# Kernel tuning notes

Hardware: AMD Instinct MI355X
Metric: run time of the kernel (lower is better)

Reference implementation:

```python
import jax, jax.numpy as jnp
import numpy as np

B, T, I, H, L = 32, 512, 512, 512, 2


def _gru_layer(x, w_ih, w_hh, b_ih, b_hh, reverse):
    # x: [B, T, in] ; w_ih: [3H, in] ; w_hh: [3H, H] ; gate order (r, z, n) as in PyTorch
    Bh = x.shape[0]
    Hh = w_hh.shape[1]
    pre = jnp.einsum('bti,gi->btg', x, w_ih) + b_ih  # [B, T, 3H] input projections, done once
    if reverse:
        pre = pre[:, ::-1]
    pre_t = jnp.swapaxes(pre, 0, 1)  # [T, B, 3H]
    h0 = jnp.zeros((Bh, Hh), x.dtype)

    def step(h, gx):
        gh = h @ w_hh.T + b_hh  # [B, 3H]
        r = jax.nn.sigmoid(gx[:, :Hh] + gh[:, :Hh])
        z = jax.nn.sigmoid(gx[:, Hh:2 * Hh] + gh[:, Hh:2 * Hh])
        n = jnp.tanh(gx[:, 2 * Hh:] + r * gh[:, 2 * Hh:])
        h_new = (1.0 - z) * n + z * h
        return h_new, h_new

    h_last, ys = jax.lax.scan(step, h0, pre_t)
    ys = jnp.swapaxes(ys, 0, 1)  # [B, T, H]
    if reverse:
        ys = ys[:, ::-1]
    return ys, h_last


def _encoder(context, params):
    # params: list of (w_ih, w_hh, b_ih, b_hh, w_ih_r, w_hh_r, b_ih_r, b_hh_r) per layer
    x = context
    finals = []  # interleaved fwd, bwd per layer, like torch GRU's `final`
    for (w_ih, w_hh, b_ih, b_hh, w_ih_r, w_hh_r, b_ih_r, b_hh_r) in params:
        y_f, h_f = _gru_layer(x, w_ih, w_hh, b_ih, b_hh, reverse=False)
        y_b, h_b = _gru_layer(x, w_ih_r, w_hh_r, b_ih_r, b_hh_r, reverse=True)
        x = jnp.concatenate([y_f, y_b], axis=-1)  # [B, T, 2H]
        finals.append(h_f)
        finals.append(h_b)
    final = jnp.stack(finals, axis=0)  # [2L, B, H]
    fwd_final = final[0::2]  # [L, B, H]
    bwd_final = final[1::2]
    final = jnp.concatenate([fwd_final, bwd_final], axis=2)  # [L, B, 2H]
    return x, final


def setup_inputs() -> dict:
    key = jax.random.key(0)
    ks = jax.random.split(key, 20)
    s = 1.0 / np.sqrt(H)  # PyTorch-style uniform-ish scale
    d = {'context': jax.random.normal(ks[0], (B, T, I), jnp.float32)}
    shapes = {
        'w_ih_l0': (3 * H, I), 'w_hh_l0': (3 * H, H), 'b_ih_l0': (3 * H,), 'b_hh_l0': (3 * H,),
        'w_ih_l0r': (3 * H, I), 'w_hh_l0r': (3 * H, H), 'b_ih_l0r': (3 * H,), 'b_hh_l0r': (3 * H,),
        'w_ih_l1': (3 * H, 2 * H), 'w_hh_l1': (3 * H, H), 'b_ih_l1': (3 * H,), 'b_hh_l1': (3 * H,),
        'w_ih_l1r': (3 * H, 2 * H), 'w_hh_l1r': (3 * H, H), 'b_ih_l1r': (3 * H,), 'b_hh_l1r': (3 * H,),
    }
    for i, (name, shp) in enumerate(shapes.items()):
        d[name] = jax.random.normal(ks[i + 1], shp, jnp.float32) * s
    return d


def reference(context, w_ih_l0, w_hh_l0, b_ih_l0, b_hh_l0,
              w_ih_l0r, w_hh_l0r, b_ih_l0r, b_hh_l0r,
              w_ih_l1, w_hh_l1, b_ih_l1, b_hh_l1,
              w_ih_l1r, w_hh_l1r, b_ih_l1r, b_hh_l1r):
    params = [
        (w_ih_l0, w_hh_l0, b_ih_l0, b_hh_l0, w_ih_l0r, w_hh_l0r, b_ih_l0r, b_hh_l0r),
        (w_ih_l1, w_hh_l1, b_ih_l1, b_hh_l1, w_ih_l1r, w_hh_l1r, b_ih_l1r, b_hh_l1r),
    ]
    return _encoder(context, params)
```

## Files before the change

### kernel.cpp

```cpp
#include <hip/hip_runtime.h>

typedef unsigned int  u32;
typedef unsigned long long u64;
typedef unsigned short u16;
typedef short s16x8 __attribute__((ext_vector_type(8)));
typedef float f32x4 __attribute__((ext_vector_type(4)));
typedef u32 u32x2 __attribute__((ext_vector_type(2)));
typedef u32 u32x4 __attribute__((ext_vector_type(4)));

#define BB 32
#define TT 512
#define HH 512
#define GG 1536
#define MM 16384

#define TAGMASK 0x4000400040004000ull

__device__ __forceinline__ u16 f2bf(float f) {
  u32 u = __builtin_bit_cast(u32, f);
  u = u + 0x7FFFu + ((u >> 16) & 1u);
  return (u16)(u >> 16);
}
__device__ __forceinline__ float bf2f(u16 h) {
  return __builtin_bit_cast(float, (u32)h << 16);
}
__device__ __forceinline__ float sigmoidf_(float x) { return 1.f / (1.f + __expf(-x)); }
__device__ __forceinline__ float tanhf_(float x)    { return 1.f - 2.f / (__expf(2.f * x) + 1.f); }

__device__ __forceinline__ u64 tagpat(u32 sig) {
  u64 t = (u64)(sig & 15u);
  return ((t & 1) << 14) | (((t >> 1) & 1) << 30) | (((t >> 2) & 1) << 46) | (((t >> 3) & 1) << 62);
}


struct PrepP {
  const float *ctx;
  const float *wih0, *whh0, *bih0, *bhh0, *wih0r, *whh0r, *bih0r, *bhh0r;
  const float *wih1, *whh1, *bih1, *bhh1, *wih1r, *whh1r, *bih1r, *bhh1r;
  u16 *a0f, *w0f, *w1f, *whh;
  float *bgx, *bhn;
  u64 *hexq;
};

__global__ void prep_kernel(PrepP P) {
  const size_t NA0 = (size_t)MM * 512;
  const size_t NW0 = (size_t)3072 * 512;
  const size_t NW1 = (size_t)3072 * 1024;
  const size_t NWH = (size_t)2 * 2 * GG * HH;
  const size_t NBG = 2 * 2 * (size_t)GG;
  const size_t NBN = 2 * 2 * (size_t)HH;
  const size_t NHX = 32768;
  const size_t TOTAL = NA0 + NW0 + NW1 + NWH + NBG + NBN + NHX;
  size_t stride = (size_t)gridDim.x * blockDim.x;
  for (size_t i = (size_t)blockIdx.x * blockDim.x + threadIdx.x; i < TOTAL; i += stride) {
    size_t e = i;
    if (e < NA0) {
      int j = e & 7, l = (e >> 3) & 63, kb = (e >> 9) & 15, mb = (int)(e >> 13);
      int m = mb * 16 + (l & 15);
      int k = kb * 32 + ((l >> 4) << 2) + (j & 3) + ((j >> 2) << 4);
      P.a0f[e] = f2bf(P.ctx[(size_t)m * 512 + k]);
      continue;
    }
    e -= NA0;
    if (e < NW0) {
      int j = e & 7, l = (e >> 3) & 63, kb = (e >> 9) & 15, nb = (int)(e >> 13);
      int n = nb * 16 + (l & 15);
      int d = (n >= GG) ? 1 : 0, g = n - d * GG;
      int k = kb * 32 + ((l >> 4) << 2) + (j & 3) + ((j >> 2) << 4);
      const float* src = d ? P.wih0r : P.wih0;
      P.w0f[e] = f2bf(src[(size_t)g * 512 + k]);
      continue;
    }
    e -= NW0;
    if (e < NW1) {
      int j = e & 7, l = (e >> 3) & 63, kb = (e >> 9) & 31, nb = (int)(e >> 14);
      int n = nb * 16 + (l & 15);
      int d = (n >= GG) ? 1 : 0, g = n - d * GG;
      int k = kb * 32 + ((l >> 4) << 2) + (j & 3) + ((j >> 2) << 4);
      const float* src = d ? P.wih1r : P.wih1;
      P.w1f[e] = f2bf(src[(size_t)g * 1024 + k]);
      continue;
    }
    e -= NW1;
    if (e < NWH) {
      size_t per = (size_t)GG * HH;
      int ld = (int)(e / per); size_t sub = e % per;
      const float* src = (ld == 0) ? P.whh0 : (ld == 1) ? P.whh0r : (ld == 2) ? P.whh1 : P.whh1r;
      P.whh[e] = f2bf(src[sub]);
      continue;
    }
    e -= NWH;
    if (e < NBG) {
      int ld = (int)(e / GG), g = (int)(e % GG);
      const float* bi = (ld == 0) ? P.bih0 : (ld == 1) ? P.bih0r : (ld == 2) ? P.bih1 : P.bih1r;
      const float* bh = (ld == 0) ? P.bhh0 : (ld == 1) ? P.bhh0r : (ld == 2) ? P.bhh1 : P.bhh1r;
      P.bgx[e] = bi[g] + ((g < 1024) ? bh[g] : 0.f);
      continue;
    }
    e -= NBG;
    if (e < NBN) {
      int ld = (int)(e / HH), u = (int)(e % HH);
      const float* bh = (ld == 0) ? P.bhh0 : (ld == 1) ? P.bhh0r : (ld == 2) ? P.bhh1 : P.bhh1r;
      P.bhn[e] = bh[1024 + u];
      continue;
    }
    e -= NBN;
    if (e < NHX) { P.hexq[e] = 0ull; continue; }
  }
}

template<bool GXF32>
__global__ __launch_bounds__(256, 2) void proj_kernel(const u16* __restrict__ A,
                                                      const u16* __restrict__ W,
                                                      void* __restrict__ gx, int KB) {
  __shared__ uint4 As4[512];
  __shared__ uint4 Bs4[512];
  const int tid = threadIdx.x;
  const int bm = blockIdx.x, bn = blockIdx.y;
  const int l = tid & 63, w = tid >> 6, wm = w >> 1, wn = w & 1;

  f32x4 acc[4][4];
#pragma unroll
  for (int i = 0; i < 4; ++i)
#pragma unroll
    for (int j = 0; j < 4; ++j) acc[i][j] = f32x4{0.f, 0.f, 0.f, 0.f};

  const uint4* GA = (const uint4*)A;
  const uint4* GB = (const uint4*)W;

  for (int kt = 0; kt < KB; ++kt) {
    __syncthreads();
#pragma unroll
    for (int c = 0; c < 2; ++c) {
      int idx = tid * 2 + c;
      int blk = idx >> 6, pos = idx & 63;
      As4[idx] = GA[((size_t)(bm * 8 + blk) * KB + kt) * 64 + pos];
      Bs4[idx] = GB[((size_t)(bn * 8 + blk) * KB + kt) * 64 + pos];
    }
    __syncthreads();
    s16x8 av[4], bv[4];
#pragma unroll
    for (int mf = 0; mf < 4; ++mf) av[mf] = ((const s16x8*)As4)[(wm * 4 + mf) * 64 + l];
#pragma unroll
    for (int nf = 0; nf < 4; ++nf) bv[nf] = ((const s16x8*)Bs4)[(wn * 4 + nf) * 64 + l];
#pragma unroll
    for (int mf = 0; mf < 4; ++mf)
#pragma unroll
      for (int nf = 0; nf < 4; ++nf)
        acc[mf][nf] = __builtin_amdgcn_mfma_f32_16x16x32_bf16(av[mf], bv[nf], acc[mf][nf], 0, 0, 0);
  }

#pragma unroll
  for (int mf = 0; mf < 4; ++mf)
#pragma unroll
    for (int nf = 0; nf < 4; ++nf)
#pragma unroll
      for (int r = 0; r < 4; ++r) {
        int m = bm * 128 + wm * 64 + mf * 16 + (l >> 4) * 4 + r;
        int n = bn * 128 + wn * 64 + nf * 16 + (l & 15);
        int b = m >> 9, t = m & 511;
        int d = (n >= GG) ? 1 : 0, g = n - d * GG;
        size_t o = ((size_t)(d * TT + t) * BB + b) * GG + g;
        float v = acc[mf][nf][r];
        if (GXF32) ((float*)gx)[o] = v;
        else       ((u16*)gx)[o] = f2bf(v);
      }
}

template<bool GXF32, bool YF32>
__global__ __launch_bounds__(256, 1) void recur_kernel(
    const void* __restrict__ gx_, const u16* __restrict__ whh,
    const float* __restrict__ bgx, const float* __restrict__ bhn_,
    void* __restrict__ yout, float* __restrict__ finals,
    u64* __restrict__ hex) {
  const int wg = blockIdx.x, d = wg >> 4, s = wg & 15;
  const int tid = threadIdx.x, l = tid & 63, w = tid >> 6;
  const int nt = w & 1, uh = w >> 1;
  const int l4 = l >> 4, lm = l & 15;
  const int b = nt * 16 + lm;
  const int u0 = s * 32 + uh * 16 + l4 * 4;

  s16x8 af[3][16];
  const u16* wd = whh + (size_t)d * (GG * HH);
#pragma unroll
  for (int g = 0; g < 3; ++g) {
    const int row = g * 512 + s * 32 + uh * 16 + lm;
    const u16* rp = wd + (size_t)row * 512 + l4 * 4;
#pragma unroll
    for (int ks = 0; ks < 16; ++ks) {
      u32 lo0 = *(const u32*)(rp + ks * 32);
      u32 lo1 = *(const u32*)(rp + ks * 32 + 2);
      u32 hi0 = *(const u32*)(rp + ks * 32 + 16);
      u32 hi1 = *(const u32*)(rp + ks * 32 + 18);
      u32x4 t4; t4.x = lo0; t4.y = lo1; t4.z = hi0; t4.w = hi1;
      af[g][ks] = __builtin_bit_cast(s16x8, t4);
    }
  }
  float bgr[4], bgz[4], bgn[4], bhn[4];
#pragma unroll
  for (int r = 0; r < 4; ++r) {
    bgr[r] = bgx[d * GG + 0 * 512 + u0 + r];
    bgz[r] = bgx[d * GG + 1 * 512 + u0 + r];
    bgn[r] = bgx[d * GG + 2 * 512 + u0 + r];
    bhn[r] = bhn_[d * HH + u0 + r];
  }
  float h[4] = {0.f, 0.f, 0.f, 0.f};

  const u32 wslot = (u32)(d * 4096 + (s * 2 + uh) * 128 + nt * 64 + l);
  const u32 rbase = (u32)(d * 4096 + nt * 64 + l);

  float gxr[4], gxz[4], gxn[4];
  {
    const int t0 = d ? 511 : 0;
    const size_t base = ((size_t)(d * TT + t0) * BB + b) * GG + u0;
    if (GXF32) {
      const float* Gp = (const float*)gx_ + base;
      f32x4 vr = *(const f32x4*)(Gp);
      f32x4 vz = *(const f32x4*)(Gp + 512);
      f32x4 vn = *(const f32x4*)(Gp + 1024);
#pragma unroll
      for (int r = 0; r < 4; ++r) { gxr[r] = vr[r]; gxz[r] = vz[r]; gxn[r] = vn[r]; }
    } else {
      const u32* Gp = (const u32*)((const u16*)gx_ + base);
      u32 vr0 = Gp[0], vr1 = Gp[1], vz0 = Gp[256], vz1 = Gp[257], vn0 = Gp[512], vn1 = Gp[513];
      gxr[0] = bf2f((u16)vr0); gxr[1] = bf2f((u16)(vr0 >> 16)); gxr[2] = bf2f((u16)vr1); gxr[3] = bf2f((u16)(vr1 >> 16));
      gxz[0] = bf2f((u16)vz0); gxz[1] = bf2f((u16)(vz0 >> 16)); gxz[2] = bf2f((u16)vz1); gxz[3] = bf2f((u16)(vz1 >> 16));
      gxn[0] = bf2f((u16)vn0); gxn[1] = bf2f((u16)(vn0 >> 16)); gxn[2] = bf2f((u16)vn1); gxn[3] = bf2f((u16)(vn1 >> 16));
    }
  }

  for (int sig = 0; sig < 512; ++sig) {
    const int t = d ? (511 - sig) : sig;

    f32x4 a0 = {0.f, 0.f, 0.f, 0.f}, a1 = a0, a2 = a0;
    if (sig > 0) {
      const u32 cb = (u32)(sig & 1) * 8192u + rbase;
      const u64 pat = tagpat((u32)sig);
      u64 v[32];
      while (true) {
#pragma unroll
        for (int q = 0; q < 32; ++q)
          v[q] = __hip_atomic_load(hex + cb + (u32)q * 128u,
                                   __ATOMIC_RELAXED, __HIP_MEMORY_SCOPE_AGENT);
        u32 good = 1u;
#pragma unroll
        for (int q = 0; q < 32; ++q)
          good &= (u32)(((v[q] ^ pat) & TAGMASK) == 0ull);
        if (__all((int)good)) break;
      }
      __builtin_amdgcn_sched_barrier(0);

#pragma unroll
      for (int ks = 0; ks < 16; ++ks) {
        u64 m0 = v[ks * 2]     & ~TAGMASK;
        u64 m1 = v[ks * 2 + 1] & ~TAGMASK;
        u32x4 t4;
        t4.x = (u32)m0; t4.y = (u32)(m0 >> 32);
        t4.z = (u32)m1; t4.w = (u32)(m1 >> 32);
        s16x8 bv = __builtin_bit_cast(s16x8, t4);
        a0 = __builtin_amdgcn_mfma_f32_16x16x32_bf16(af[0][ks], bv, a0, 0, 0, 0);
        a1 = __builtin_amdgcn_mfma_f32_16x16x32_bf16(af[1][ks], bv, a1, 0, 0, 0);
        a2 = __builtin_amdgcn_mfma_f32_16x16x32_bf16(af[2][ks], bv, a2, 0, 0, 0);
      }
    }

    u16 hb16[4];
#pragma unroll
    for (int r = 0; r < 4; ++r) {
      float rr = sigmoidf_(gxr[r] + bgr[r] + a0[r]);
      float zz = sigmoidf_(gxz[r] + bgz[r] + a1[r]);
      float nn = tanhf_(gxn[r] + bgn[r] + rr * (a2[r] + bhn[r]));
      h[r] = (1.f - zz) * nn + zz * h[r];
      hb16[r] = f2bf(h[r]);
    }
    u32 pk0 = (u32)hb16[0] | ((u32)hb16[1] << 16);
    u32 pk1 = (u32)hb16[2] | ((u32)hb16[3] << 16);

    if (sig < 511) {
      u64 pk = ((u64)pk0 | ((u64)pk1 << 32)) | tagpat((u32)(sig + 1));
      __hip_atomic_store(hex + (u32)((sig + 1) & 1) * 8192u + wslot, pk,
                         __ATOMIC_RELAXED, __HIP_MEMORY_SCOPE_AGENT);
    }

    if (YF32) {
      f32x4 yv; yv.x = h[0]; yv.y = h[1]; yv.z = h[2]; yv.w = h[3];
      *(f32x4*)((float*)yout + ((size_t)(b * TT + t) * 1024 + d * 512 + u0)) = yv;
    } else {
      size_t o = (((size_t)(b * 32 + (t >> 4)) * 32 + (d * 16 + s)) * 64 + (l4 * 16 + (t & 15))) * 8 + 4 * uh;
      u32x2 pk; pk.x = pk0; pk.y = pk1;
      *(u32x2*)((u16*)yout + o) = pk;
    }
    if (sig == 511) {
      f32x4 fv; fv.x = h[0]; fv.y = h[1]; fv.z = h[2]; fv.w = h[3];
      *(f32x4*)(finals + (size_t)b * 1024 + d * 512 + u0) = fv;
      break;
    }

    {
      const int t2 = d ? (511 - (sig + 1)) : (sig + 1);
      const size_t base = ((size_t)(d * TT + t2) * BB + b) * GG + u0;
      if (GXF32) {
        const float* Gp = (const float*)gx_ + base;
        f32x4 vr = *(const f32x4*)(Gp);
        f32x4 vz = *(const f32x4*)(Gp + 512);
        f32x4 vn = *(const f32x4*)(Gp + 1024);
#pragma unroll
        for (int r = 0; r < 4; ++r) { gxr[r] = vr[r]; gxz[r] = vz[r]; gxn[r] = vn[r]; }
      } else {
        const u32* Gp = (const u32*)((const u16*)gx_ + base);
        u32 vr0 = Gp[0], vr1 = Gp[1], vz0 = Gp[256], vz1 = Gp[257], vn0 = Gp[512], vn1 = Gp[513];
        gxr[0] = bf2f((u16)vr0); gxr[1] = bf2f((u16)(vr0 >> 16)); gxr[2] = bf2f((u16)vr1); gxr[3] = bf2f((u16)(vr1 >> 16));
        gxz[0] = bf2f((u16)vz0); gxz[1] = bf2f((u16)(vz0 >> 16)); gxz[2] = bf2f((u16)vz1); gxz[3] = bf2f((u16)(vz1 >> 16));
        gxn[0] = bf2f((u16)vn0); gxn[1] = bf2f((u16)(vn0 >> 16)); gxn[2] = bf2f((u16)vn1); gxn[3] = bf2f((u16)(vn1 >> 16));
      }
    }
  }
}

extern "C" void kernel_launch(void* const* d_in, const int* in_sizes, int n_in,
                              void* d_out, int out_size, void* d_ws, size_t ws_size,
                              hipStream_t stream) {
  (void)in_sizes; (void)n_in; (void)out_size;
  const float* ctx   = (const float*)d_in[0];
  const float* wih0  = (const float*)d_in[1];
  const float* whh0  = (const float*)d_in[2];
  const float* bih0  = (const float*)d_in[3];
  const float* bhh0  = (const float*)d_in[4];
  const float* wih0r = (const float*)d_in[5];
  const float* whh0r = (const float*)d_in[6];
  const float* bih0r = (const float*)d_in[7];
  const float* bhh0r = (const float*)d_in[8];
  const float* wih1  = (const float*)d_in[9];
  const float* whh1  = (const float*)d_in[10];
  const float* bih1  = (const float*)d_in[11];
  const float* bhh1  = (const float*)d_in[12];
  const float* wih1r = (const float*)d_in[13];
  const float* whh1r = (const float*)d_in[14];
  const float* bih1r = (const float*)d_in[15];
  const float* bhh1r = (const float*)d_in[16];

  char* ws = (char*)d_ws;
  size_t off = 0;
  auto take = [&](size_t bytes) { char* p = ws + off; off += bytes; return p; };
  u16*   a0f  = (u16*)take(16777216);
  u16*   a1f  = (u16*)take(33554432);
  u16*   w0f  = (u16*)take(3145728);
  u16*   w1f  = (u16*)take(6291456);
  u16*   whhb = (u16*)take(6291456);
  float* bgx  = (float*)take(24576);
  float* bhn  = (float*)take(8192);
  u64*   hexA = (u64*)take(131072);
  u64*   hexB = (u64*)take(131072);
  const size_t GXF32_BYTES = 201326592;
  const size_t GXB16_BYTES = 100663296;
  bool gxf32 = (ws_size >= off + GXF32_BYTES);
  void* gx = (void*)take(gxf32 ? GXF32_BYTES : GXB16_BYTES);

  PrepP P;
  P.ctx = ctx;
  P.wih0 = wih0; P.whh0 = whh0; P.bih0 = bih0; P.bhh0 = bhh0;
  P.wih0r = wih0r; P.whh0r = whh0r; P.bih0r = bih0r; P.bhh0r = bhh0r;
  P.wih1 = wih1; P.whh1 = whh1; P.bih1 = bih1; P.bhh1 = bhh1;
  P.wih1r = wih1r; P.whh1r = whh1r; P.bih1r = bih1r; P.bhh1r = bhh1r;
  P.a0f = a0f; P.w0f = w0f; P.w1f = w1f; P.whh = whhb;
  P.bgx = bgx; P.bhn = bhn; P.hexq = hexA;

  prep_kernel<<<dim3(2048), dim3(256), 0, stream>>>(P);

  float* fin = (float*)d_out + (size_t)MM * 1024;
  if (gxf32) {
    proj_kernel<true><<<dim3(128, 24), dim3(256), 0, stream>>>(a0f, w0f, gx, 16);
    recur_kernel<true, false><<<dim3(32), dim3(256), 0, stream>>>(
        gx, whhb, bgx, bhn, a1f, fin, hexA);
    proj_kernel<true><<<dim3(128, 24), dim3(256), 0, stream>>>(a1f, w1f, gx, 32);
    recur_kernel<true, true><<<dim3(32), dim3(256), 0, stream>>>(
        gx, whhb + (size_t)2 * GG * HH, bgx + 2 * GG, bhn + 2 * HH, d_out, fin + 32768, hexB);
  } else {
    proj_kernel<false><<<dim3(128, 24), dim3(256), 0, stream>>>(a0f, w0f, gx, 16);
    recur_kernel<false, false><<<dim3(32), dim3(256), 0, stream>>>(
        gx, whhb, bgx, bhn, a1f, fin, hexA);
    proj_kernel<false><<<dim3(128, 24), dim3(256), 0, stream>>>(a1f, w1f, gx, 32);
    recur_kernel<false, true><<<dim3(32), dim3(256), 0, stream>>>(
        gx, whhb + (size_t)2 * GG * HH, bgx + 2 * GG, bhn + 2 * HH, d_out, fin + 32768, hexB);
  }
}
```

Measured before the change: 3.022 ms.

## Poll only unready hidden-state slots and split MFMA accumulation chains

The spin-wait on the tagged hidden-state exchange buffer now reloads only the slots whose tag is not yet valid, instead of reloading all 32 on every retry. Readiness is tracked per slot with a wave-wide vote and a bitmask. The recurrent matmul is also split into two independent accumulator chains over the K range, summed at the end, so fewer MFMAs depend on each other in sequence. The cost is more registers for the extra accumulators, more divergent control flow in the poll loop, and a slightly different floating-point summation order.

```diff
diff --git a/kernel.cpp b/kernel.cpp
--- a/kernel.cpp
+++ b/kernel.cpp
@@ -233,25 +233,35 @@
     const int t = d ? (511 - sig) : sig;
 
     f32x4 a0 = {0.f, 0.f, 0.f, 0.f}, a1 = a0, a2 = a0;
+    f32x4 a0b = a0, a1b = a0, a2b = a0;
     if (sig > 0) {
       const u32 cb = (u32)(sig & 1) * 8192u + rbase;
       const u64 pat = tagpat((u32)sig);
       u64 v[32];
+      u32 goodmask = 0u;
+#pragma unroll
+      for (int q = 0; q < 32; ++q)
+        v[q] = __hip_atomic_load(hex + cb + (u32)q * 128u,
+                                 __ATOMIC_RELAXED, __HIP_MEMORY_SCOPE_AGENT);
       while (true) {
 #pragma unroll
-        for (int q = 0; q < 32; ++q)
-          v[q] = __hip_atomic_load(hex + cb + (u32)q * 128u,
-                                   __ATOMIC_RELAXED, __HIP_MEMORY_SCOPE_AGENT);
-        u32 good = 1u;
-#pragma unroll
-        for (int q = 0; q < 32; ++q)
-          good &= (u32)(((v[q] ^ pat) & TAGMASK) == 0ull);
-        if (__all((int)good)) break;
+        for (int q = 0; q < 32; ++q) {
+          if (!((goodmask >> q) & 1u)) {
+            if (__all(((v[q] ^ pat) & TAGMASK) == 0ull)) goodmask |= (1u << q);
+          }
+        }
+        if (goodmask == 0xFFFFFFFFu) break;
+#pragma unroll
+        for (int q = 0; q < 32; ++q) {
+          if (!((goodmask >> q) & 1u))
+            v[q] = __hip_atomic_load(hex + cb + (u32)q * 128u,
+                                     __ATOMIC_RELAXED, __HIP_MEMORY_SCOPE_AGENT);
+        }
       }
       __builtin_amdgcn_sched_barrier(0);
 
 #pragma unroll
-      for (int ks = 0; ks < 16; ++ks) {
+      for (int ks = 0; ks < 8; ++ks) {
         u64 m0 = v[ks * 2]     & ~TAGMASK;
         u64 m1 = v[ks * 2 + 1] & ~TAGMASK;
         u32x4 t4;
@@ -262,6 +272,20 @@
         a1 = __builtin_amdgcn_mfma_f32_16x16x32_bf16(af[1][ks], bv, a1, 0, 0, 0);
         a2 = __builtin_amdgcn_mfma_f32_16x16x32_bf16(af[2][ks], bv, a2, 0, 0, 0);
       }
+#pragma unroll
+      for (int ks = 8; ks < 16; ++ks) {
+        u64 m0 = v[ks * 2]     & ~TAGMASK;
+        u64 m1 = v[ks * 2 + 1] & ~TAGMASK;
+        u32x4 t4;
+        t4.x = (u32)m0; t4.y = (u32)(m0 >> 32);
+        t4.z = (u32)m1; t4.w = (u32)(m1 >> 32);
+        s16x8 bv = __builtin_bit_cast(s16x8, t4);
+        a0b = __builtin_amdgcn_mfma_f32_16x16x32_bf16(af[0][ks], bv, a0b, 0, 0, 0);
+        a1b = __builtin_amdgcn_mfma_f32_16x16x32_bf16(af[1][ks], bv, a1b, 0, 0, 0);
+        a2b = __builtin_amdgcn_mfma_f32_16x16x32_bf16(af[2][ks], bv, a2b, 0, 0, 0);
+      }
+#pragma unroll
+      for (int r = 0; r < 4; ++r) { a0[r] += a0b[r]; a1[r] += a1b[r]; a2[r] += a2b[r]; }
     }
 
     u16 hb16[4];
```

Result: slower. 4.250 ms (+40.6%).
